# Performance work log

Measured on AMD Instinct MI355X. Metric: run time of the kernel, lower is better.

## Reference

```python
import jax, jax.numpy as jnp
import numpy as np

V, D, H, HD, L, F, T, B = 1024, 768, 12, 64, 8, 3072, 1024, 2
STD = 0.02
EPS = 1e-5


def setup_inputs() -> dict:
    key = jax.random.key(0)
    ks = jax.random.split(key, 8)
    n = jax.random.normal
    return {
        "input_ids": jax.random.randint(ks[0], (B, T), 0, V),
        "tok_emb": n(ks[1], (V, D), dtype=jnp.float32) * STD,   # tied with lm_head
        "pos_emb": n(ks[2], (1, T, D), dtype=jnp.float32) * STD,
        "ln1_w": jnp.ones((L, D)), "ln1_b": jnp.zeros((L, D)),
        "qkv_w": n(ks[3], (L, D, 3 * D), dtype=jnp.float32) * STD,
        "out_w": n(ks[4], (L, D, D), dtype=jnp.float32) * STD,
        "ln2_w": jnp.ones((L, D)), "ln2_b": jnp.zeros((L, D)),
        "ffn_w1": n(ks[5], (L, D, F), dtype=jnp.float32) * STD,
        "ffn_b1": jnp.zeros((L, F)),
        "ffn_w2": n(ks[6], (L, F, D), dtype=jnp.float32) * STD,
        "ffn_b2": jnp.zeros((L, D)),
        "lnf_w": jnp.ones((D,)), "lnf_b": jnp.zeros((D,)),
    }


def _layernorm(x, w, b):
    mu = x.mean(-1, keepdims=True)
    var = ((x - mu) ** 2).mean(-1, keepdims=True)
    return (x - mu) * jax.lax.rsqrt(var + EPS) * w + b


def _forward(input_ids, tok_emb, pos_emb, ln1_w, ln1_b, qkv_w, out_w,
             ln2_w, ln2_b, ffn_w1, ffn_b1, ffn_w2, ffn_b2, lnf_w, lnf_b):
    x = tok_emb[input_ids] + pos_emb[:, :T, :]          # (B, T, D)
    causal = jnp.tril(jnp.ones((T, T), dtype=bool))     # (T, T)
    neg_inf = jnp.finfo(x.dtype).min

    def block(x, p):
        l1w, l1b, qkvw, ow, l2w, l2b, w1, b1, w2, b2 = p
        h = _layernorm(x, l1w, l1b)
        qkv = h @ qkvw                                   # (B, T, 3D)
        q, k, v = jnp.split(qkv, 3, axis=-1)
        q = q.reshape(B, T, H, HD).transpose(0, 2, 1, 3)  # (B, H, T, HD)
        k = k.reshape(B, T, H, HD).transpose(0, 2, 1, 3)
        v = v.reshape(B, T, H, HD).transpose(0, 2, 1, 3)
        att = jnp.einsum('bhqd,bhkd->bhqk', q, k) * (1.0 / np.sqrt(HD))
        att = jnp.where(causal, att, neg_inf)
        att = jax.nn.softmax(att, axis=-1)
        y = jnp.einsum('bhqk,bhkd->bhqd', att, v)        # (B, H, T, HD)
        y = y.transpose(0, 2, 1, 3).reshape(B, T, D)
        x = x + y @ ow
        h = _layernorm(x, l2w, l2b)
        x = x + jax.nn.gelu(h @ w1 + b1, approximate=False) @ w2 + b2
        return x, None

    params = (ln1_w, ln1_b, qkv_w, out_w, ln2_w, ln2_b,
              ffn_w1, ffn_b1, ffn_w2, ffn_b2)
    x, _ = jax.lax.scan(block, x, params)
    x = _layernorm(x, lnf_w, lnf_b)
    return x @ tok_emb.T                                 # tied lm_head -> (B, T, V)


def reference(input_ids, tok_emb, pos_emb, ln1_w, ln1_b, qkv_w, out_w,
              ln2_w, ln2_b, ffn_w1, ffn_b1, ffn_w2, ffn_b2, lnf_w, lnf_b):
    return _forward(input_ids, tok_emb, pos_emb, ln1_w, ln1_b, qkv_w, out_w,
                    ln2_w, ln2_b, ffn_w1, ffn_b1, ffn_w2, ffn_b2, lnf_w, lnf_b)
```

## Files before the change

kernel.cpp:

```cpp
#include <hip/hip_runtime.h>
#include <hip/hip_bf16.h>
#include <math.h>

#define D_  768
#define T_  1024
#define B_  2
#define H_  12
#define HD_ 64
#define L_  8
#define F_  3072
#define V_  1024
#define M_  (B_ * T_)

typedef __bf16 bf16_t;
typedef __bf16 bf16x8 __attribute__((ext_vector_type(8)));
typedef float  f32x4  __attribute__((ext_vector_type(4)));

__device__ __forceinline__ void ld_g2l16(const bf16_t* g, bf16_t* l)
{
    __builtin_amdgcn_global_load_lds(
        (const __attribute__((address_space(1))) void*)g,
        (__attribute__((address_space(3))) void*)l,
        16, 0, 0);
}

__global__ __launch_bounds__(256) void embed_kernel(
    const int* __restrict__ ids, const float* __restrict__ tok,
    const float* __restrict__ pos, float* __restrict__ x)
{
    const int row = blockIdx.x;
    const int t   = row & (T_ - 1);
    const int id  = ids[row];
    const int c   = threadIdx.x;
#pragma unroll
    for (int i = 0; i < 3; ++i) {
        const int d = c + i * 256;
        x[(size_t)row * D_ + d] = tok[(size_t)id * D_ + d] + pos[(size_t)t * D_ + d];
    }
}

__global__ __launch_bounds__(256) void wtrans_kernel(
    const float* __restrict__ in, bf16_t* __restrict__ out, int K, int N)
{
    __shared__ float tile[32][33];
    const int n0 = blockIdx.x * 32, k0 = blockIdx.y * 32;
    const int tx = threadIdx.x & 31, ty = threadIdx.x >> 5;
#pragma unroll
    for (int i = 0; i < 4; ++i)
        tile[ty + 8 * i][tx] = in[(size_t)(k0 + ty + 8 * i) * N + n0 + tx];
    __syncthreads();
#pragma unroll
    for (int i = 0; i < 4; ++i) {
        const int n = ty + 8 * i;
        out[(size_t)(n0 + n) * K + k0 + tx] = (bf16_t)tile[tx][n];
    }
}

__global__ __launch_bounds__(256) void conv_kernel(
    const float* __restrict__ in, bf16_t* __restrict__ out)
{
    const int i = blockIdx.x * 1024 + threadIdx.x * 4;
    const f32x4 v = *(const f32x4*)(in + i);
#pragma unroll
    for (int j = 0; j < 4; ++j) out[i + j] = (bf16_t)v[j];
}

__device__ __forceinline__ float block_sum(float v)
{
    __shared__ float sm[4];
#pragma unroll
    for (int off = 32; off; off >>= 1) v += __shfl_down(v, off);
    if ((threadIdx.x & 63) == 0) sm[threadIdx.x >> 6] = v;
    __syncthreads();
    const float r = sm[0] + sm[1] + sm[2] + sm[3];
    __syncthreads();
    return r;
}

__global__ __launch_bounds__(256) void ln_kernel(
    const float* __restrict__ x, const float* __restrict__ w,
    const float* __restrict__ b, bf16_t* __restrict__ out)
{
    const int row = blockIdx.x;
    const float* xr = x + (size_t)row * D_;
    const int t = threadIdx.x;
    const float v0 = xr[t];
    const float v1 = xr[t + 256];
    const float v2 = xr[t + 512];
    const float mu = block_sum(v0 + v1 + v2) * (1.f / D_);
    const float d0 = v0 - mu, d1 = v1 - mu, d2 = v2 - mu;
    const float var = block_sum(d0 * d0 + d1 * d1 + d2 * d2) * (1.f / D_);
    const float rstd = rsqrtf(var + 1e-5f);
    bf16_t* o = out + (size_t)row * D_;
    o[t]       = (bf16_t)(d0 * rstd * w[t]       + b[t]);
    o[t + 256] = (bf16_t)(d1 * rstd * w[t + 256] + b[t + 256]);
    o[t + 512] = (bf16_t)(d2 * rstd * w[t + 512] + b[t + 512]);
}

template<int BN, bool RES, bool BIAS, bool GELU_, bool OUTF32>
__global__ __launch_bounds__(256) void gemm_bt(
    const bf16_t* __restrict__ A, const bf16_t* __restrict__ Bt,
    const float* __restrict__ bias, const float* __restrict__ res,
    void* __restrict__ Cp, int M, int N, int K)
{
    constexpr int BM = 64, BK = 64;
    constexpr int WN = BN / 2, NT = WN / 16;
    constexpr int AR = (BM * BK) / (256 * 8);
    constexpr int BR = (BN * BK) / (256 * 8);
    __shared__ bf16_t As[BM * BK];
    __shared__ bf16_t Bs[BN * BK];

    const int t    = threadIdx.x;
    const int wave = t >> 6, lane = t & 63;
    const int lr   = lane & 15, quad = lane >> 4;
    const int bm0  = blockIdx.y * BM, bn0 = blockIdx.x * BN;
    const int wm   = wave >> 1, wn = wave & 1;

    f32x4 acc[2][NT];
#pragma unroll
    for (int i = 0; i < 2; ++i)
#pragma unroll
        for (int j = 0; j < NT; ++j) { f32x4 z = {0.f, 0.f, 0.f, 0.f}; acc[i][j] = z; }

    const bf16_t* asrc[AR];
    const bf16_t* bsrc[BR];
#pragma unroll
    for (int rnd = 0; rnd < AR; ++rnd) {
        const int p = rnd * 256 + t, row = p >> 3, c = (p & 7) ^ (row & 7);
        asrc[rnd] = A + (size_t)(bm0 + row) * K + c * 8;
    }
#pragma unroll
    for (int rnd = 0; rnd < BR; ++rnd) {
        const int p = rnd * 256 + t, row = p >> 3, c = (p & 7) ^ (row & 7);
        bsrc[rnd] = Bt + (size_t)(bn0 + row) * K + c * 8;
    }

    for (int k0 = 0; k0 < K; k0 += BK) {
        __syncthreads();
#pragma unroll
        for (int rnd = 0; rnd < AR; ++rnd)
            ld_g2l16(asrc[rnd] + k0, As + (rnd * 256 + wave * 64) * 8);
#pragma unroll
        for (int rnd = 0; rnd < BR; ++rnd)
            ld_g2l16(bsrc[rnd] + k0, Bs + (rnd * 256 + wave * 64) * 8);
        __syncthreads();

#pragma unroll
        for (int ks = 0; ks < 2; ++ks) {
            const int ch = ((quad + 4 * ks) ^ (lr & 7)) * 8;
            const bf16x8 a0 = *(const bf16x8*)(As + (wm * 32 + lr) * BK + ch);
            const bf16x8 a1 = *(const bf16x8*)(As + (wm * 32 + 16 + lr) * BK + ch);
#pragma unroll
            for (int nt = 0; nt < NT; ++nt) {
                const bf16x8 b = *(const bf16x8*)(Bs + (wn * WN + nt * 16 + lr) * BK + ch);
                acc[0][nt] = __builtin_amdgcn_mfma_f32_16x16x32_bf16(a0, b, acc[0][nt], 0, 0, 0);
                acc[1][nt] = __builtin_amdgcn_mfma_f32_16x16x32_bf16(a1, b, acc[1][nt], 0, 0, 0);
            }
        }
    }

#pragma unroll
    for (int mt = 0; mt < 2; ++mt) {
        const int mbase = bm0 + wm * 32 + mt * 16 + quad * 4;
#pragma unroll
        for (int nt = 0; nt < NT; ++nt) {
            const int n = bn0 + wn * WN + nt * 16 + lr;
            const float bv = BIAS ? bias[n] : 0.f;
#pragma unroll
            for (int r = 0; r < 4; ++r) {
                const int m = mbase + r;
                float v = acc[mt][nt][r] + bv;
                if (RES)   v += res[(size_t)m * N + n];
                if (GELU_) v = 0.5f * v * (1.f + erff(v * 0.70710678118654752f));
                if (OUTF32) ((float*)Cp)[(size_t)m * N + n] = v;
                else        ((bf16_t*)Cp)[(size_t)m * N + n] = (bf16_t)v;
            }
        }
    }
}

__global__ __launch_bounds__(256) void attn_kernel(
    const bf16_t* __restrict__ qkv, bf16_t* __restrict__ y)
{
    __shared__ bf16_t Ks[64][72];
    __shared__ bf16_t Vt[64][72];
    __shared__ bf16_t Ps[4][16][72];

    const int q0   = blockIdx.x * 64;
    const int bh   = blockIdx.y;
    const int b    = bh / H_;
    const int hh   = bh % H_;
    const int t    = threadIdx.x;
    const int wave = t >> 6;
    const int lane = t & 63;
    const int lr   = lane & 15;
    const int quad = lane >> 4;

    const size_t qg = ((size_t)b * T_ + q0 + wave * 16 + lr) * (3 * D_) + hh * HD_;
    const bf16x8 aQ0 = *(const bf16x8*)(qkv + qg + quad * 8);
    const bf16x8 aQ1 = *(const bf16x8*)(qkv + qg + 32 + quad * 8);

    const size_t rowb  = (size_t)b * T_;
    const size_t tstep = (size_t)64 * 3 * D_;
    const int    kkey  = t >> 2, kdc = (t & 3) * 8;
    const bf16_t* kptr = qkv + (rowb + kkey) * (3 * D_) + D_ + hh * HD_ + kdc;
    const bf16_t* vptr = qkv + (rowb + lane) * (3 * D_) + 2 * D_ + hh * HD_ + wave * 16;

    bf16x8 rk0 = *(const bf16x8*)(kptr);
    bf16x8 rk1 = *(const bf16x8*)(kptr + 32);
    bf16x8 rv0 = *(const bf16x8*)(vptr);
    bf16x8 rv1 = *(const bf16x8*)(vptr + 8);

    f32x4 o[4];
#pragma unroll
    for (int i = 0; i < 4; ++i) { f32x4 z = {0.f, 0.f, 0.f, 0.f}; o[i] = z; }
    float mrow[4] = {-1e30f, -1e30f, -1e30f, -1e30f};
    float lrow[4] = {0.f, 0.f, 0.f, 0.f};

    for (int kt = 0; kt <= (int)blockIdx.x; ++kt) {
        const int k_base = kt * 64;
        __syncthreads();

        *(bf16x8*)(&Ks[kkey][kdc])      = rk0;
        *(bf16x8*)(&Ks[kkey][kdc + 32]) = rk1;
#pragma unroll
        for (int i = 0; i < 8; ++i) {
            Vt[wave * 16 + i][lane]     = rv0[i];
            Vt[wave * 16 + 8 + i][lane] = rv1[i];
        }
        __syncthreads();

        if (kt < (int)blockIdx.x) {
            const bf16_t* kp = kptr + (size_t)(kt + 1) * tstep;
            const bf16_t* vp = vptr + (size_t)(kt + 1) * tstep;
            rk0 = *(const bf16x8*)(kp);
            rk1 = *(const bf16x8*)(kp + 32);
            rv0 = *(const bf16x8*)(vp);
            rv1 = *(const bf16x8*)(vp + 8);
        }

        f32x4 s[4];
#pragma unroll
        for (int i = 0; i < 4; ++i) { f32x4 z = {0.f, 0.f, 0.f, 0.f}; s[i] = z; }
#pragma unroll
        for (int nt = 0; nt < 4; ++nt) {
            bf16x8 bk0 = *(const bf16x8*)(&Ks[nt * 16 + lr][quad * 8]);
            bf16x8 bk1 = *(const bf16x8*)(&Ks[nt * 16 + lr][32 + quad * 8]);
            s[nt] = __builtin_amdgcn_mfma_f32_16x16x32_bf16(aQ0, bk0, s[nt], 0, 0, 0);
            s[nt] = __builtin_amdgcn_mfma_f32_16x16x32_bf16(aQ1, bk1, s[nt], 0, 0, 0);
        }

#pragma unroll
        for (int r = 0; r < 4; ++r) {
            const int qg_i = q0 + wave * 16 + quad * 4 + r;
            float mx = -1e30f;
#pragma unroll
            for (int nt = 0; nt < 4; ++nt) {
                float sv = s[nt][r] * 0.125f;
                if (k_base + nt * 16 + lr > qg_i) sv = -1e30f;
                s[nt][r] = sv;
                mx = fmaxf(mx, sv);
            }
            mx = fmaxf(mx, __shfl_xor(mx, 1));
            mx = fmaxf(mx, __shfl_xor(mx, 2));
            mx = fmaxf(mx, __shfl_xor(mx, 4));
            mx = fmaxf(mx, __shfl_xor(mx, 8));
            const float mnew = fmaxf(mrow[r], mx);
            float ps = 0.f;
#pragma unroll
            for (int nt = 0; nt < 4; ++nt) {
                const float p = __expf(s[nt][r] - mnew);
                s[nt][r] = p;
                ps += p;
            }
            ps += __shfl_xor(ps, 1);
            ps += __shfl_xor(ps, 2);
            ps += __shfl_xor(ps, 4);
            ps += __shfl_xor(ps, 8);
            const float alpha = __expf(mrow[r] - mnew);
            lrow[r] = lrow[r] * alpha + ps;
            mrow[r] = mnew;
#pragma unroll
            for (int nt = 0; nt < 4; ++nt) o[nt][r] *= alpha;
        }

#pragma unroll
        for (int nt = 0; nt < 4; ++nt)
#pragma unroll
            for (int r = 0; r < 4; ++r)
                Ps[wave][quad * 4 + r][nt * 16 + lr] = (bf16_t)s[nt][r];

        const bf16x8 aP0 = *(const bf16x8*)(&Ps[wave][lr][quad * 8]);
        const bf16x8 aP1 = *(const bf16x8*)(&Ps[wave][lr][32 + quad * 8]);
#pragma unroll
        for (int nt = 0; nt < 4; ++nt) {
            bf16x8 bv0 = *(const bf16x8*)(&Vt[nt * 16 + lr][quad * 8]);
            bf16x8 bv1 = *(const bf16x8*)(&Vt[nt * 16 + lr][32 + quad * 8]);
            o[nt] = __builtin_amdgcn_mfma_f32_16x16x32_bf16(aP0, bv0, o[nt], 0, 0, 0);
            o[nt] = __builtin_amdgcn_mfma_f32_16x16x32_bf16(aP1, bv1, o[nt], 0, 0, 0);
        }
    }

#pragma unroll
    for (int r = 0; r < 4; ++r) {
        const float inv = 1.f / lrow[r];
        const size_t row = (size_t)b * T_ + q0 + wave * 16 + quad * 4 + r;
#pragma unroll
        for (int nt = 0; nt < 4; ++nt)
            y[row * D_ + hh * HD_ + nt * 16 + lr] = (bf16_t)(o[nt][r] * inv);
    }
}

extern "C" void kernel_launch(void* const* d_in, const int* in_sizes, int n_in,
                              void* d_out, int out_size, void* d_ws, size_t ws_size,
                              hipStream_t stream)
{
    const int*   ids  = (const int*)d_in[0];
    const float* tok  = (const float*)d_in[1];
    const float* pos  = (const float*)d_in[2];
    const float* l1w  = (const float*)d_in[3];
    const float* l1b  = (const float*)d_in[4];
    const float* qkvw = (const float*)d_in[5];
    const float* outw = (const float*)d_in[6];
    const float* l2w  = (const float*)d_in[7];
    const float* l2b  = (const float*)d_in[8];
    const float* w1   = (const float*)d_in[9];
    const float* b1   = (const float*)d_in[10];
    const float* w2   = (const float*)d_in[11];
    const float* b2   = (const float*)d_in[12];
    const float* lnfw = (const float*)d_in[13];
    const float* lnfb = (const float*)d_in[14];

    float*  x     = (float*)d_ws;
    bf16_t* h     = (bf16_t*)(x + (size_t)M_ * D_);
    bf16_t* qkv   = h     + (size_t)M_ * D_;
    bf16_t* y     = qkv   + (size_t)M_ * 3 * D_;
    bf16_t* mid   = y     + (size_t)M_ * D_;
    bf16_t* tokb  = mid   + (size_t)M_ * F_;
    bf16_t* wqkvT = tokb  + (size_t)V_ * D_;
    bf16_t* woutT = wqkvT + (size_t)3 * D_ * D_;
    bf16_t* w1T   = woutT + (size_t)D_ * D_;
    bf16_t* w2T   = w1T   + (size_t)F_ * D_;

    embed_kernel<<<M_, 256, 0, stream>>>(ids, tok, pos, x);
    conv_kernel<<<(V_ * D_) / 1024, 256, 0, stream>>>(tok, tokb);

    for (int l = 0; l < L_; ++l) {
        wtrans_kernel<<<dim3(3 * D_ / 32, D_ / 32), 256, 0, stream>>>(
            qkvw + (size_t)l * D_ * 3 * D_, wqkvT, D_, 3 * D_);
        wtrans_kernel<<<dim3(D_ / 32, D_ / 32), 256, 0, stream>>>(
            outw + (size_t)l * D_ * D_, woutT, D_, D_);
        wtrans_kernel<<<dim3(F_ / 32, D_ / 32), 256, 0, stream>>>(
            w1 + (size_t)l * D_ * F_, w1T, D_, F_);
        wtrans_kernel<<<dim3(D_ / 32, F_ / 32), 256, 0, stream>>>(
            w2 + (size_t)l * F_ * D_, w2T, F_, D_);

        ln_kernel<<<M_, 256, 0, stream>>>(x, l1w + l * D_, l1b + l * D_, h);
        gemm_bt<128, false, false, false, false><<<dim3(3 * D_ / 128, M_ / 64), 256, 0, stream>>>(
            h, wqkvT, nullptr, nullptr, qkv, M_, 3 * D_, D_);
        attn_kernel<<<dim3(T_ / 64, B_ * H_), 256, 0, stream>>>(qkv, y);
        gemm_bt<64, true, false, false, true><<<dim3(D_ / 64, M_ / 64), 256, 0, stream>>>(
            y, woutT, nullptr, x, x, M_, D_, D_);
        ln_kernel<<<M_, 256, 0, stream>>>(x, l2w + l * D_, l2b + l * D_, h);
        gemm_bt<128, false, true, true, false><<<dim3(F_ / 128, M_ / 64), 256, 0, stream>>>(
            h, w1T, b1 + (size_t)l * F_, nullptr, mid, M_, F_, D_);
        gemm_bt<64, true, true, false, true><<<dim3(D_ / 64, M_ / 64), 256, 0, stream>>>(
            mid, w2T, b2 + (size_t)l * D_, x, x, M_, D_, F_);
    }

    ln_kernel<<<M_, 256, 0, stream>>>(x, lnfw, lnfb, h);
    gemm_bt<64, false, false, false, true><<<dim3(V_ / 64, M_ / 64), 256, 0, stream>>>(
        h, tokb, nullptr, nullptr, d_out, M_, V_, D_);
}
```

Before: 1.327 ms.

## Batch weight transposes, add 128x128 GEMM tile, reverse attention block order

```diff
diff --git a/kernel.cpp b/kernel.cpp
--- a/kernel.cpp
+++ b/kernel.cpp
@@ -43,16 +43,19 @@
     const float* __restrict__ in, bf16_t* __restrict__ out, int K, int N)
 {
     __shared__ float tile[32][33];
+    const size_t loff = (size_t)blockIdx.z * K * N;
+    const float* inp  = in  + loff;
+    bf16_t*      outp = out + loff;
     const int n0 = blockIdx.x * 32, k0 = blockIdx.y * 32;
     const int tx = threadIdx.x & 31, ty = threadIdx.x >> 5;
 #pragma unroll
     for (int i = 0; i < 4; ++i)
-        tile[ty + 8 * i][tx] = in[(size_t)(k0 + ty + 8 * i) * N + n0 + tx];
+        tile[ty + 8 * i][tx] = inp[(size_t)(k0 + ty + 8 * i) * N + n0 + tx];
     __syncthreads();
 #pragma unroll
     for (int i = 0; i < 4; ++i) {
         const int n = ty + 8 * i;
-        out[(size_t)(n0 + n) * K + k0 + tx] = (bf16_t)tile[tx][n];
+        outp[(size_t)(n0 + n) * K + k0 + tx] = (bf16_t)tile[tx][n];
     }
 }
 
@@ -179,6 +182,81 @@
     }
 }
 
+template<bool BIAS, bool GELU_>
+__global__ __launch_bounds__(256) void gemm_bt128(
+    const bf16_t* __restrict__ A, const bf16_t* __restrict__ Bt,
+    const float* __restrict__ bias, bf16_t* __restrict__ C,
+    int M, int N, int K)
+{
+    constexpr int BM = 128, BN = 128, BK = 64;
+    __shared__ bf16_t As[BM * BK];
+    __shared__ bf16_t Bs[BN * BK];
+
+    const int t    = threadIdx.x;
+    const int wave = t >> 6, lane = t & 63;
+    const int lr   = lane & 15, quad = lane >> 4;
+    const int bm0  = blockIdx.y * BM, bn0 = blockIdx.x * BN;
+    const int wm   = wave >> 1, wn = wave & 1;
+
+    f32x4 acc[4][4];
+#pragma unroll
+    for (int i = 0; i < 4; ++i)
+#pragma unroll
+        for (int j = 0; j < 4; ++j) { f32x4 z = {0.f, 0.f, 0.f, 0.f}; acc[i][j] = z; }
+
+    const bf16_t* asrc[4];
+    const bf16_t* bsrc[4];
+#pragma unroll
+    for (int rnd = 0; rnd < 4; ++rnd) {
+        const int p = rnd * 256 + t, row = p >> 3, c = (p & 7) ^ (row & 7);
+        asrc[rnd] = A  + (size_t)(bm0 + row) * K + c * 8;
+        bsrc[rnd] = Bt + (size_t)(bn0 + row) * K + c * 8;
+    }
+
+    for (int k0 = 0; k0 < K; k0 += BK) {
+        __syncthreads();
+#pragma unroll
+        for (int rnd = 0; rnd < 4; ++rnd)
+            ld_g2l16(asrc[rnd] + k0, As + (rnd * 256 + wave * 64) * 8);
+#pragma unroll
+        for (int rnd = 0; rnd < 4; ++rnd)
+            ld_g2l16(bsrc[rnd] + k0, Bs + (rnd * 256 + wave * 64) * 8);
+        __syncthreads();
+
+#pragma unroll
+        for (int ks = 0; ks < 2; ++ks) {
+            const int ch = ((quad + 4 * ks) ^ (lr & 7)) * 8;
+            bf16x8 a[4];
+#pragma unroll
+            for (int mt = 0; mt < 4; ++mt)
+                a[mt] = *(const bf16x8*)(As + (wm * 64 + mt * 16 + lr) * BK + ch);
+#pragma unroll
+            for (int nt = 0; nt < 4; ++nt) {
+                const bf16x8 b = *(const bf16x8*)(Bs + (wn * 64 + nt * 16 + lr) * BK + ch);
+#pragma unroll
+                for (int mt = 0; mt < 4; ++mt)
+                    acc[mt][nt] = __builtin_amdgcn_mfma_f32_16x16x32_bf16(a[mt], b, acc[mt][nt], 0, 0, 0);
+            }
+        }
+    }
+
+#pragma unroll
+    for (int mt = 0; mt < 4; ++mt) {
+        const int mbase = bm0 + wm * 64 + mt * 16 + quad * 4;
+#pragma unroll
+        for (int nt = 0; nt < 4; ++nt) {
+            const int n = bn0 + wn * 64 + nt * 16 + lr;
+            const float bv = BIAS ? bias[n] : 0.f;
+#pragma unroll
+            for (int r = 0; r < 4; ++r) {
+                float v = acc[mt][nt][r] + bv;
+                if (GELU_) v = 0.5f * v * (1.f + erff(v * 0.70710678118654752f));
+                C[(size_t)(mbase + r) * N + n] = (bf16_t)v;
+            }
+        }
+    }
+}
+
 __global__ __launch_bounds__(256) void attn_kernel(
     const bf16_t* __restrict__ qkv, bf16_t* __restrict__ y)
 {
@@ -186,7 +264,8 @@
     __shared__ bf16_t Vt[64][72];
     __shared__ bf16_t Ps[4][16][72];
 
-    const int q0   = blockIdx.x * 64;
+    const int qt   = (int)gridDim.x - 1 - (int)blockIdx.x;
+    const int q0   = qt * 64;
     const int bh   = blockIdx.y;
     const int b    = bh / H_;
     const int hh   = bh % H_;
@@ -217,7 +296,7 @@
     float mrow[4] = {-1e30f, -1e30f, -1e30f, -1e30f};
     float lrow[4] = {0.f, 0.f, 0.f, 0.f};
 
-    for (int kt = 0; kt <= (int)blockIdx.x; ++kt) {
+    for (int kt = 0; kt <= qt; ++kt) {
         const int k_base = kt * 64;
         __syncthreads();
 
@@ -230,7 +309,7 @@
         }
         __syncthreads();
 
-        if (kt < (int)blockIdx.x) {
+        if (kt < qt) {
             const bf16_t* kp = kptr + (size_t)(kt + 1) * tstep;
             const bf16_t* vp = vptr + (size_t)(kt + 1) * tstep;
             rk0 = *(const bf16x8*)(kp);
@@ -338,34 +417,35 @@
     bf16_t* mid   = y     + (size_t)M_ * D_;
     bf16_t* tokb  = mid   + (size_t)M_ * F_;
     bf16_t* wqkvT = tokb  + (size_t)V_ * D_;
-    bf16_t* woutT = wqkvT + (size_t)3 * D_ * D_;
-    bf16_t* w1T   = woutT + (size_t)D_ * D_;
-    bf16_t* w2T   = w1T   + (size_t)F_ * D_;
+    bf16_t* woutT = wqkvT + (size_t)L_ * 3 * D_ * D_;
+    bf16_t* w1T   = woutT + (size_t)L_ * D_ * D_;
+    bf16_t* w2T   = w1T   + (size_t)L_ * D_ * F_;
 
     embed_kernel<<<M_, 256, 0, stream>>>(ids, tok, pos, x);
     conv_kernel<<<(V_ * D_) / 1024, 256, 0, stream>>>(tok, tokb);
 
+    wtrans_kernel<<<dim3(3 * D_ / 32, D_ / 32, L_), 256, 0, stream>>>(qkvw, wqkvT, D_, 3 * D_);
+    wtrans_kernel<<<dim3(D_ / 32, D_ / 32, L_), 256, 0, stream>>>(outw, woutT, D_, D_);
+    wtrans_kernel<<<dim3(F_ / 32, D_ / 32, L_), 256, 0, stream>>>(w1, w1T, D_, F_);
+    wtrans_kernel<<<dim3(D_ / 32, F_ / 32, L_), 256, 0, stream>>>(w2, w2T, F_, D_);
+
     for (int l = 0; l < L_; ++l) {
-        wtrans_kernel<<<dim3(3 * D_ / 32, D_ / 32), 256, 0, stream>>>(
-            qkvw + (size_t)l * D_ * 3 * D_, wqkvT, D_, 3 * D_);
-        wtrans_kernel<<<dim3(D_ / 32, D_ / 32), 256, 0, stream>>>(
-            outw + (size_t)l * D_ * D_, woutT, D_, D_);
-        wtrans_kernel<<<dim3(F_ / 32, D_ / 32), 256, 0, stream>>>(
-            w1 + (size_t)l * D_ * F_, w1T, D_, F_);
-        wtrans_kernel<<<dim3(D_ / 32, F_ / 32), 256, 0, stream>>>(
-            w2 + (size_t)l * F_ * D_, w2T, F_, D_);
+        const bf16_t* wq = wqkvT + (size_t)l * 3 * D_ * D_;
+        const bf16_t* wo = woutT + (size_t)l * D_ * D_;
+        const bf16_t* wf1 = w1T + (size_t)l * D_ * F_;
+        const bf16_t* wf2 = w2T + (size_t)l * F_ * D_;
 
         ln_kernel<<<M_, 256, 0, stream>>>(x, l1w + l * D_, l1b + l * D_, h);
-        gemm_bt<128, false, false, false, false><<<dim3(3 * D_ / 128, M_ / 64), 256, 0, stream>>>(
-            h, wqkvT, nullptr, nullptr, qkv, M_, 3 * D_, D_);
+        gemm_bt128<false, false><<<dim3(3 * D_ / 128, M_ / 128), 256, 0, stream>>>(
+            h, wq, nullptr, qkv, M_, 3 * D_, D_);
         attn_kernel<<<dim3(T_ / 64, B_ * H_), 256, 0, stream>>>(qkv, y);
         gemm_bt<64, true, false, false, true><<<dim3(D_ / 64, M_ / 64), 256, 0, stream>>>(
-            y, woutT, nullptr, x, x, M_, D_, D_);
+            y, wo, nullptr, x, x, M_, D_, D_);
         ln_kernel<<<M_, 256, 0, stream>>>(x, l2w + l * D_, l2b + l * D_, h);
-        gemm_bt<128, false, true, true, false><<<dim3(F_ / 128, M_ / 64), 256, 0, stream>>>(
-            h, w1T, b1 + (size_t)l * F_, nullptr, mid, M_, F_, D_);
+        gemm_bt128<true, true><<<dim3(F_ / 128, M_ / 128), 256, 0, stream>>>(
+            h, wf1, b1 + (size_t)l * F_, mid, M_, F_, D_);
         gemm_bt<64, true, true, false, true><<<dim3(D_ / 64, M_ / 64), 256, 0, stream>>>(
-            mid, w2T, b2 + (size_t)l * D_, x, x, M_, D_, F_);
+            mid, wf2, b2 + (size_t)l * D_, x, x, M_, D_, F_);
     }
 
     ln_kernel<<<M_, 256, 0, stream>>>(x, lnfw, lnfb, h);
```

New measurement: 1.394 ms. +5.1%, slower.

## Batch weight transposes, remap GEMM tiles per XCD, reverse attention order, DPP reductions

Applied to the files above, without the earlier changes.

```diff
diff --git a/kernel.cpp b/kernel.cpp
--- a/kernel.cpp
+++ b/kernel.cpp
@@ -24,6 +24,30 @@
         16, 0, 0);
 }
 
+template<int CTRL>
+__device__ __forceinline__ float dpp_f32(float v)
+{
+    return __builtin_bit_cast(float,
+        __builtin_amdgcn_update_dpp(0, __builtin_bit_cast(int, v),
+                                    CTRL, 0xf, 0xf, true));
+}
+__device__ __forceinline__ float red16_max(float v)
+{
+    v = fmaxf(v, dpp_f32<0x121>(v));
+    v = fmaxf(v, dpp_f32<0x122>(v));
+    v = fmaxf(v, dpp_f32<0x124>(v));
+    v = fmaxf(v, dpp_f32<0x128>(v));
+    return v;
+}
+__device__ __forceinline__ float red16_sum(float v)
+{
+    v += dpp_f32<0x121>(v);
+    v += dpp_f32<0x122>(v);
+    v += dpp_f32<0x124>(v);
+    v += dpp_f32<0x128>(v);
+    return v;
+}
+
 __global__ __launch_bounds__(256) void embed_kernel(
     const int* __restrict__ ids, const float* __restrict__ tok,
     const float* __restrict__ pos, float* __restrict__ x)
@@ -43,16 +67,19 @@
     const float* __restrict__ in, bf16_t* __restrict__ out, int K, int N)
 {
     __shared__ float tile[32][33];
+    const size_t loff = (size_t)blockIdx.z * K * N;
+    const float* inp  = in  + loff;
+    bf16_t*      outp = out + loff;
     const int n0 = blockIdx.x * 32, k0 = blockIdx.y * 32;
     const int tx = threadIdx.x & 31, ty = threadIdx.x >> 5;
 #pragma unroll
     for (int i = 0; i < 4; ++i)
-        tile[ty + 8 * i][tx] = in[(size_t)(k0 + ty + 8 * i) * N + n0 + tx];
+        tile[ty + 8 * i][tx] = inp[(size_t)(k0 + ty + 8 * i) * N + n0 + tx];
     __syncthreads();
 #pragma unroll
     for (int i = 0; i < 4; ++i) {
         const int n = ty + 8 * i;
-        out[(size_t)(n0 + n) * K + k0 + tx] = (bf16_t)tile[tx][n];
+        outp[(size_t)(n0 + n) * K + k0 + tx] = (bf16_t)tile[tx][n];
     }
 }
 
@@ -113,7 +140,13 @@
     const int t    = threadIdx.x;
     const int wave = t >> 6, lane = t & 63;
     const int lr   = lane & 15, quad = lane >> 4;
-    const int bm0  = blockIdx.y * BM, bn0 = blockIdx.x * BN;
+
+    const int nx  = gridDim.x;
+    const int nwg = nx * gridDim.y;
+    int id = blockIdx.y * nx + blockIdx.x;
+    id = (id & 7) * (nwg >> 3) + (id >> 3);
+    const int bn0 = (id % nx) * BN, bm0 = (id / nx) * BM;
+
     const int wm   = wave >> 1, wn = wave & 1;
 
     f32x4 acc[2][NT];
@@ -186,7 +219,8 @@
     __shared__ bf16_t Vt[64][72];
     __shared__ bf16_t Ps[4][16][72];
 
-    const int q0   = blockIdx.x * 64;
+    const int qt   = (int)gridDim.x - 1 - (int)blockIdx.x;
+    const int q0   = qt * 64;
     const int bh   = blockIdx.y;
     const int b    = bh / H_;
     const int hh   = bh % H_;
@@ -217,7 +251,7 @@
     float mrow[4] = {-1e30f, -1e30f, -1e30f, -1e30f};
     float lrow[4] = {0.f, 0.f, 0.f, 0.f};
 
-    for (int kt = 0; kt <= (int)blockIdx.x; ++kt) {
+    for (int kt = 0; kt <= qt; ++kt) {
         const int k_base = kt * 64;
         __syncthreads();
 
@@ -230,7 +264,7 @@
         }
         __syncthreads();
 
-        if (kt < (int)blockIdx.x) {
+        if (kt < qt) {
             const bf16_t* kp = kptr + (size_t)(kt + 1) * tstep;
             const bf16_t* vp = vptr + (size_t)(kt + 1) * tstep;
             rk0 = *(const bf16x8*)(kp);
@@ -261,10 +295,7 @@
                 s[nt][r] = sv;
                 mx = fmaxf(mx, sv);
             }
-            mx = fmaxf(mx, __shfl_xor(mx, 1));
-            mx = fmaxf(mx, __shfl_xor(mx, 2));
-            mx = fmaxf(mx, __shfl_xor(mx, 4));
-            mx = fmaxf(mx, __shfl_xor(mx, 8));
+            mx = red16_max(mx);
             const float mnew = fmaxf(mrow[r], mx);
             float ps = 0.f;
 #pragma unroll
@@ -273,10 +304,7 @@
                 s[nt][r] = p;
                 ps += p;
             }
-            ps += __shfl_xor(ps, 1);
-            ps += __shfl_xor(ps, 2);
-            ps += __shfl_xor(ps, 4);
-            ps += __shfl_xor(ps, 8);
+            ps = red16_sum(ps);
             const float alpha = __expf(mrow[r] - mnew);
             lrow[r] = lrow[r] * alpha + ps;
             mrow[r] = mnew;
@@ -338,34 +366,35 @@
     bf16_t* mid   = y     + (size_t)M_ * D_;
     bf16_t* tokb  = mid   + (size_t)M_ * F_;
     bf16_t* wqkvT = tokb  + (size_t)V_ * D_;
-    bf16_t* woutT = wqkvT + (size_t)3 * D_ * D_;
-    bf16_t* w1T   = woutT + (size_t)D_ * D_;
-    bf16_t* w2T   = w1T   + (size_t)F_ * D_;
+    bf16_t* woutT = wqkvT + (size_t)L_ * 3 * D_ * D_;
+    bf16_t* w1T   = woutT + (size_t)L_ * D_ * D_;
+    bf16_t* w2T   = w1T   + (size_t)L_ * D_ * F_;
 
     embed_kernel<<<M_, 256, 0, stream>>>(ids, tok, pos, x);
     conv_kernel<<<(V_ * D_) / 1024, 256, 0, stream>>>(tok, tokb);
 
+    wtrans_kernel<<<dim3(3 * D_ / 32, D_ / 32, L_), 256, 0, stream>>>(qkvw, wqkvT, D_, 3 * D_);
+    wtrans_kernel<<<dim3(D_ / 32, D_ / 32, L_), 256, 0, stream>>>(outw, woutT, D_, D_);
+    wtrans_kernel<<<dim3(F_ / 32, D_ / 32, L_), 256, 0, stream>>>(w1, w1T, D_, F_);
+    wtrans_kernel<<<dim3(D_ / 32, F_ / 32, L_), 256, 0, stream>>>(w2, w2T, F_, D_);
+
     for (int l = 0; l < L_; ++l) {
-        wtrans_kernel<<<dim3(3 * D_ / 32, D_ / 32), 256, 0, stream>>>(
-            qkvw + (size_t)l * D_ * 3 * D_, wqkvT, D_, 3 * D_);
-        wtrans_kernel<<<dim3(D_ / 32, D_ / 32), 256, 0, stream>>>(
-            outw + (size_t)l * D_ * D_, woutT, D_, D_);
-        wtrans_kernel<<<dim3(F_ / 32, D_ / 32), 256, 0, stream>>>(
-            w1 + (size_t)l * D_ * F_, w1T, D_, F_);
-        wtrans_kernel<<<dim3(D_ / 32, F_ / 32), 256, 0, stream>>>(
-            w2 + (size_t)l * F_ * D_, w2T, F_, D_);
+        const bf16_t* wq  = wqkvT + (size_t)l * 3 * D_ * D_;
+        const bf16_t* wo  = woutT + (size_t)l * D_ * D_;
+        const bf16_t* wf1 = w1T   + (size_t)l * D_ * F_;
+        const bf16_t* wf2 = w2T   + (size_t)l * F_ * D_;
 
         ln_kernel<<<M_, 256, 0, stream>>>(x, l1w + l * D_, l1b + l * D_, h);
         gemm_bt<128, false, false, false, false><<<dim3(3 * D_ / 128, M_ / 64), 256, 0, stream>>>(
-            h, wqkvT, nullptr, nullptr, qkv, M_, 3 * D_, D_);
+            h, wq, nullptr, nullptr, qkv, M_, 3 * D_, D_);
         attn_kernel<<<dim3(T_ / 64, B_ * H_), 256, 0, stream>>>(qkv, y);
         gemm_bt<64, true, false, false, true><<<dim3(D_ / 64, M_ / 64), 256, 0, stream>>>(
-            y, woutT, nullptr, x, x, M_, D_, D_);
+            y, wo, nullptr, x, x, M_, D_, D_);
         ln_kernel<<<M_, 256, 0, stream>>>(x, l2w + l * D_, l2b + l * D_, h);
         gemm_bt<128, false, true, true, false><<<dim3(F_ / 128, M_ / 64), 256, 0, stream>>>(
-            h, w1T, b1 + (size_t)l * F_, nullptr, mid, M_, F_, D_);
+            h, wf1, b1 + (size_t)l * F_, nullptr, mid, M_, F_, D_);
         gemm_bt<64, true, true, false, true><<<dim3(D_ / 64, M_ / 64), 256, 0, stream>>>(
-            mid, w2T, b2 + (size_t)l * D_, x, x, M_, D_, F_);
+            mid, wf2, b2 + (size_t)l * D_, x, x, M_, D_, F_);
     }
 
     ln_kernel<<<M_, 256, 0, stream>>>(x, lnfw, lnfb, h);
```

Result: faster. 1.255 ms (-5.4%).
